# Performance work log

Measured on AMD Instinct MI355X. Metric: run time of the kernel, lower is better.

Reference implementation:

```python
import jax, jax.numpy as jnp
import numpy as np

B, T, E, H, D_PRICE = 16, 2048, 128, 4, 512


def setup_inputs() -> dict:
    key = jax.random.key(0)
    ks = jax.random.split(key, 22)
    f32 = jnp.float32

    def w(k, shape):
        fan_in = shape[0]
        return (jax.random.normal(k, shape, f32) / np.sqrt(fan_in)).astype(f32)

    def b(k, n):
        return (jax.random.normal(k, (n,), f32) * 0.01).astype(f32)

    inp = {
        # OHLC prices, positive, normalized scale
        "ohlc": jax.random.uniform(ks[0], (B, T, 4), f32, 0.5, 1.5),
        # ohlc_proj: Linear(4, 64)
        "Wp": w(ks[1], (4, 64)), "bp": b(ks[2], 64),
        # curvature_net: Linear(64,128) -> ReLU -> Linear(128,32)
        "Wc1": w(ks[3], (64, 128)), "bc1": b(ks[4], 128),
        "Wc2": w(ks[5], (128, 32)), "bc2": b(ks[6], 32),
        # volatility_net: Linear(64,64) -> ReLU -> Linear(64,16)
        "Wv1": w(ks[7], (64, 64)), "bv1": b(ks[8], 64),
        "Wv2": w(ks[9], (64, 16)), "bv2": b(ks[10], 16),
        # sr_field_net: Linear(64,64) -> ReLU -> Linear(64,16)
        "Ws1": w(ks[11], (64, 64)), "bs1": b(ks[12], 64),
        "Ws2": w(ks[13], (64, 16)), "bs2": b(ks[14], 16),
        # MultiheadAttention(embed_dim=128, num_heads=4): fused in-proj + out-proj
        "Wqkv": w(ks[15], (E, 3 * E)), "bqkv": b(ks[16], 3 * E),
        "Wo": w(ks[17], (E, E)), "bo": b(ks[18], E),
        # output_proj: Linear(128, d_price)
        "Wout": w(ks[19], (E, D_PRICE)), "bout": b(ks[20], D_PRICE),
    }
    return inp


def _mlp(x, W1, b1, W2, b2):
    return jax.nn.relu(x @ W1 + b1) @ W2 + b2


def reference(ohlc, Wp, bp, Wc1, bc1, Wc2, bc2, Wv1, bv1, Wv2, bv2,
              Ws1, bs1, Ws2, bs2, Wqkv, bqkv, Wo, bo, Wout, bout):
    # NB: compute_curvature / compute_volatility_surface / detect_sr_levels
    # in the original forward are dead code (results never used), so they are
    # omitted here; output math is identical.
    e = ohlc @ Wp + bp                                   # [B,T,64]
    feats = jnp.concatenate([
        e,
        _mlp(e, Wc1, bc1, Wc2, bc2),                     # [B,T,32]
        _mlp(e, Wv1, bv1, Wv2, bv2),                     # [B,T,16]
        _mlp(e, Ws1, bs1, Ws2, bs2),                     # [B,T,16]
    ], axis=-1)                                          # [B,T,128]

    Bn, Tn, En = feats.shape
    dh = En // H
    qkv = feats @ Wqkv + bqkv                            # [B,T,3E]
    q, k, v = jnp.split(qkv, 3, axis=-1)

    def heads(x):
        return x.reshape(Bn, Tn, H, dh).transpose(0, 2, 1, 3)  # [B,H,T,dh]

    q, k, v = heads(q), heads(k), heads(v)
    scores = jnp.einsum('bhqd,bhkd->bhqk', q, k) / np.sqrt(dh).astype(feats.dtype)
    a = jax.nn.softmax(scores, axis=-1)                  # [B,H,T,T]
    o = jnp.einsum('bhqk,bhkd->bhqd', a, v)
    o = o.transpose(0, 2, 1, 3).reshape(Bn, Tn, En)
    attended = o @ Wo + bo                               # [B,T,128]

    pooled = attended.mean(axis=1)                       # [B,128]
    return pooled @ Wout + bout                          # [B,512]
```

## Files before the change

kernel.cpp:

```cpp
#include <hip/hip_runtime.h>


typedef __attribute__((ext_vector_type(4)))  float f32x4;
typedef __attribute__((ext_vector_type(16))) float f32x16;
typedef __attribute__((ext_vector_type(4)))  short short4v;
typedef __attribute__((ext_vector_type(8)))  short short8v;

static __device__ __forceinline__ unsigned short f2b(float f) {
    unsigned int u = __builtin_bit_cast(unsigned int, f);
    u += 0x7fffu + ((u >> 16) & 1u);
    return (unsigned short)(u >> 16);
}

static __device__ __forceinline__ unsigned int cvtpk_bf16(float a, float b) {
    unsigned int r;
    asm volatile("v_cvt_pk_bf16_f32 %0, %1, %2" : "=v"(r) : "v"(a), "v"(b));
    return r;
}

__global__ __launch_bounds__(256) void prep_kernel(
    const float* Wqkv, const float* Wc1, const float* Wc2, const float* Wv1,
    const float* Wv2, const float* Ws1, const float* Ws2,
    unsigned short* wqkvt, unsigned short* wc1t, unsigned short* wc2t,
    unsigned short* wv1t, unsigned short* wv2t, unsigned short* ws1t,
    unsigned short* ws2t, float* pooled, float* qkmax)
{
    int tid = threadIdx.x;
    if (blockIdx.x < 48) {
        __shared__ float tile[32][33];
        int bidn = blockIdx.x % 12, bidk = blockIdx.x / 12;
        int n0 = bidn * 32, k0 = bidk * 32;
        {
            int r = tid >> 3, cq = tid & 7;
            float4 v = *(const float4*)(Wqkv + (size_t)(k0 + r) * 384 + n0 + cq * 4);
            tile[r][cq*4+0] = v.x; tile[r][cq*4+1] = v.y;
            tile[r][cq*4+2] = v.z; tile[r][cq*4+3] = v.w;
        }
        __syncthreads();
        {
            int nr = tid >> 3, kq = tid & 7;
            union { unsigned short us[4]; short4v v; } pk;
#pragma unroll
            for (int j = 0; j < 4; ++j) pk.us[j] = f2b(tile[kq*4+j][nr]);
            *(short4v*)(wqkvt + (size_t)(n0 + nr) * 128 + k0 + kq * 4) = pk.v;
        }
        return;
    }
    int idx = (blockIdx.x - 48) * 256 + tid;
    if (idx < 8192)  { int n = idx >> 6, kk = idx & 63;  wc1t[idx] = f2b(Wc1[kk*128 + n]); return; }
    idx -= 8192;
    if (idx < 4096)  { int n = idx >> 7, kk = idx & 127; wc2t[idx] = f2b(Wc2[kk*32  + n]); return; }
    idx -= 4096;
    if (idx < 4096)  { int n = idx >> 6, kk = idx & 63;  wv1t[idx] = f2b(Wv1[kk*64  + n]); return; }
    idx -= 4096;
    if (idx < 1024)  { int n = idx >> 6, kk = idx & 63;  wv2t[idx] = f2b(Wv2[kk*16  + n]); return; }
    idx -= 1024;
    if (idx < 4096)  { int n = idx >> 6, kk = idx & 63;  ws1t[idx] = f2b(Ws1[kk*64  + n]); return; }
    idx -= 4096;
    if (idx < 1024)  { int n = idx >> 6, kk = idx & 63;  ws2t[idx] = f2b(Ws2[kk*16  + n]); return; }
    idx -= 1024;
    if (idx < 2048)  { pooled[idx] = 0.f; return; }
    idx -= 2048;
    if (idx < 128)   qkmax[idx] = 0.f;
}

template<int N, int K, int A_ROWB, bool RELU, bool TO_LDS>
static __device__ __forceinline__ void tile_gemm(
    const char* As, const unsigned short* __restrict__ BT,
    const float* __restrict__ bias, char* Ht,
    unsigned short* __restrict__ gOut, int ocol,
    int m0, int w, int lane)
{
    constexpr int ASL = A_ROWB / 16, NT = N / 16, KS = K / 32;
    int l15 = lane & 15, hi4 = lane >> 4;
    f32x4 acc[NT];
#pragma unroll
    for (int nt = 0; nt < NT; ++nt)
#pragma unroll
        for (int r = 0; r < 4; ++r) acc[nt][r] = 0.f;

#pragma unroll
    for (int ks = 0; ks < KS; ++ks) {
        int slot = ks * 4 + hi4;
        int m = w * 16 + l15;
        short8v af = *(const short8v*)(As + m * A_ROWB + ((slot ^ (m & (ASL - 1))) << 4));
#pragma unroll
        for (int nt = 0; nt < NT; ++nt) {
            int n = nt * 16 + l15;
            short8v bf = *(const short8v*)(BT + (size_t)n * K + slot * 8);
            acc[nt] = __builtin_amdgcn_mfma_f32_16x16x32_bf16(af, bf, acc[nt], 0, 0, 0);
        }
    }
#pragma unroll
    for (int nt = 0; nt < NT; ++nt) {
        int n = nt * 16 + l15;
        float bv = bias[n];
#pragma unroll
        for (int r = 0; r < 4; ++r) {
            int m = w * 16 + hi4 * 4 + r;
            float v = acc[nt][r] + bv;
            if (RELU) v = fmaxf(v, 0.f);
            if (TO_LDS) {
                *(unsigned short*)(Ht + m * 256 + ((((n >> 3) ^ (m & 15))) << 4) + (n & 7) * 2) = f2b(v);
            } else {
                gOut[(size_t)(m0 + m) * 128 + ocol + n] = f2b(v);
            }
        }
    }
}

__global__ __launch_bounds__(256) void fused_mlp(
    const float* __restrict__ ohlc, const float* __restrict__ Wp, const float* __restrict__ bp,
    const unsigned short* __restrict__ wc1t, const float* __restrict__ bc1,
    const unsigned short* __restrict__ wc2t, const float* __restrict__ bc2,
    const unsigned short* __restrict__ wv1t, const float* __restrict__ bv1,
    const unsigned short* __restrict__ wv2t, const float* __restrict__ bv2,
    const unsigned short* __restrict__ ws1t, const float* __restrict__ bs1,
    const unsigned short* __restrict__ ws2t, const float* __restrict__ bs2,
    unsigned short* __restrict__ feats)
{
    __shared__ float wp[256];
    __shared__ float bpl[64];
    __shared__ char Et[64 * 128];
    __shared__ char Ht[64 * 256];

    int tid = threadIdx.x;
    int m0 = blockIdx.x * 64;
    wp[tid] = Wp[tid];
    if (tid < 64) bpl[tid] = bp[tid];
    __syncthreads();

    {
        int tok = tid >> 2, jq = tid & 3;
        float4 ov = ((const float4*)ohlc)[m0 + tok];
#pragma unroll
        for (int c = 0; c < 2; ++c) {
            int sl = jq * 2 + c;
            union { unsigned short us[8]; short8v v; } pk;
#pragma unroll
            for (int jj = 0; jj < 8; ++jj) {
                int j = sl * 8 + jj;
                float e = bpl[j] + ov.x * wp[j] + ov.y * wp[64 + j]
                                 + ov.z * wp[128 + j] + ov.w * wp[192 + j];
                pk.us[jj] = f2b(e);
            }
            *(short8v*)(Et + tok * 128 + ((sl ^ (tok & 7)) << 4)) = pk.v;
            *(short8v*)(feats + (size_t)(m0 + tok) * 128 + sl * 8) = pk.v;
        }
    }
    __syncthreads();

    int lane = tid & 63, w = tid >> 6;
    tile_gemm<128, 64, 128, true,  true >(Et, wc1t, bc1, Ht, feats, 0,   m0, w, lane);
    tile_gemm<32, 128, 256, false, false>(Ht, wc2t, bc2, Ht, feats, 64,  m0, w, lane);
    tile_gemm<64,  64, 128, true,  true >(Et, wv1t, bv1, Ht, feats, 0,   m0, w, lane);
    tile_gemm<16,  64, 256, false, false>(Ht, wv2t, bv2, Ht, feats, 96,  m0, w, lane);
    tile_gemm<64,  64, 128, true,  true >(Et, ws1t, bs1, Ht, feats, 0,   m0, w, lane);
    tile_gemm<16,  64, 256, false, false>(Ht, ws2t, bs2, Ht, feats, 112, m0, w, lane);
}

__global__ __launch_bounds__(256) void qkv_gemm(
    const unsigned short* __restrict__ feats,
    const unsigned short* __restrict__ wqkvt, const float* __restrict__ bqkv,
    unsigned short* __restrict__ qg, unsigned short* __restrict__ kg,
    unsigned short* __restrict__ vt2, float* __restrict__ qkmax)
{
    constexpr int ROWB = 256, CPR = 16;
    __shared__ short8v smemv[4096];
    char* As = (char*)smemv;
    char* Bs = (char*)smemv + 32768;

    int tid = threadIdx.x;
    int m0 = blockIdx.x * 128;
    int sel = blockIdx.y;
    const unsigned short* BT = wqkvt + (size_t)sel * 128 * 128;

    for (int c = tid; c < 128 * CPR; c += 256) {
        int m = c / CPR, s = c % CPR;
        short8v v = *(const short8v*)(feats + (size_t)(m0 + m) * 128 + s * 8);
        *(short8v*)(As + m * ROWB + ((s ^ (m & 15)) * 16)) = v;
    }
    for (int c = tid; c < 128 * CPR; c += 256) {
        int n = c / CPR, s = c % CPR;
        short8v v = *(const short8v*)(BT + (size_t)n * 128 + s * 8);
        *(short8v*)(Bs + n * ROWB + ((s ^ (n & 15)) * 16)) = v;
    }
    __syncthreads();

    int lane = tid & 63, w = tid >> 6;
    int l15 = lane & 15, hi4 = lane >> 4;

    f32x4 acc[2][8];
#pragma unroll
    for (int mt = 0; mt < 2; ++mt)
#pragma unroll
        for (int nt = 0; nt < 8; ++nt)
#pragma unroll
            for (int r = 0; r < 4; ++r) acc[mt][nt][r] = 0.f;

#pragma unroll
    for (int ks = 0; ks < 4; ++ks) {
        int slot = ks * 4 + hi4;
        short8v af[2];
#pragma unroll
        for (int mt = 0; mt < 2; ++mt) {
            int m = w * 32 + mt * 16 + l15;
            af[mt] = *(const short8v*)(As + m * ROWB + ((slot ^ (m & 15)) * 16));
        }
#pragma unroll
        for (int nt = 0; nt < 8; ++nt) {
            int n = nt * 16 + l15;
            short8v bf = *(const short8v*)(Bs + n * ROWB + ((slot ^ (n & 15)) * 16));
            acc[0][nt] = __builtin_amdgcn_mfma_f32_16x16x32_bf16(af[0], bf, acc[0][nt], 0, 0, 0);
            acc[1][nt] = __builtin_amdgcn_mfma_f32_16x16x32_bf16(af[1], bf, acc[1][nt], 0, 0, 0);
        }
    }

    const float QSCALE = 1.4426950408889634f * 0.17677669529663687f;
    int b = m0 >> 11, tp0 = m0 & 2047;

    if (sel == 2) {
#pragma unroll
        for (int mt = 0; mt < 2; ++mt)
#pragma unroll
            for (int nt = 0; nt < 8; ++nt) {
                int n = nt * 16 + l15;
                float bv = bqkv[256 + n];
                int h = n >> 5, dh = n & 31;
                uint2 pk;
                pk.x = cvtpk_bf16(acc[mt][nt][0] + bv, acc[mt][nt][1] + bv);
                pk.y = cvtpk_bf16(acc[mt][nt][2] + bv, acc[mt][nt][3] + bv);
                int g32 = (tp0 >> 5) + w;
                size_t o = (size_t)(b * 4 + h) * 65536 + (size_t)g32 * 1024
                         + dh * 32 + hi4 * 8 + mt * 4;
                *(uint2*)(vt2 + o) = pk;
            }
    } else {
        float amax[4] = {0.f, 0.f, 0.f, 0.f};
        float scale = (sel == 0) ? QSCALE : 1.0f;
#pragma unroll
        for (int mt = 0; mt < 2; ++mt)
#pragma unroll
            for (int nt = 0; nt < 8; ++nt) {
                int n = nt * 16 + l15;
                float bv = bqkv[sel * 128 + n];
#pragma unroll
                for (int r = 0; r < 4; ++r) {
                    float v = (acc[mt][nt][r] + bv) * scale;
                    amax[nt >> 1] = fmaxf(amax[nt >> 1], fabsf(v));
                    int m = w * 32 + mt * 16 + hi4 * 4 + r;
                    *(unsigned short*)(As + m * 256 + (((n >> 3) ^ (m & 7)) << 4) + (n & 7) * 2) = f2b(v);
                }
            }
#pragma unroll
        for (int g = 0; g < 4; ++g) {
            float mv = amax[g];
            mv = fmaxf(mv, __shfl_xor(mv, 1));  mv = fmaxf(mv, __shfl_xor(mv, 2));
            mv = fmaxf(mv, __shfl_xor(mv, 4));  mv = fmaxf(mv, __shfl_xor(mv, 8));
            mv = fmaxf(mv, __shfl_xor(mv, 16)); mv = fmaxf(mv, __shfl_xor(mv, 32));
            if (lane == 0)
                atomicMax((int*)(qkmax + sel * 64 + b * 4 + g), __float_as_int(mv));
        }
        __syncthreads();
        unsigned short* og = (sel == 0) ? qg : kg;
#pragma unroll
        for (int it = 0; it < 8; ++it) {
            int ch = it * 256 + tid;
            int m = ch >> 4, c = ch & 15;
            short8v vv = *(const short8v*)(As + m * 256 + ((c ^ (m & 7)) << 4));
            int h = c >> 2, dq = c & 3;
            *(short8v*)(og + ((size_t)(b * 4 + h) * 2048 + tp0 + m) * 32 + dq * 8) = vv;
        }
    }
}

__global__ __launch_bounds__(256, 2) void attn_kernel(
    const unsigned short* __restrict__ qg, const unsigned short* __restrict__ kg,
    const unsigned short* __restrict__ vt2, const float* __restrict__ qkmax,
    float* __restrict__ pooled)
{
    int tid = threadIdx.x, bid = blockIdx.x;
    int bh = bid & 63, qc = bid >> 6;
    int b = bh >> 2;
    int lane = tid & 63, w = tid >> 6;
    int l15 = lane & 15, h = (lane >> 4) & 3;
    int q0 = qc * 256 + w * 64;

    const char* qp = (const char*)qg + ((size_t)bh * 2048 + q0) * 64 + l15 * 64 + h * 16;
    short8v Qf[4];
#pragma unroll
    for (int j = 0; j < 4; ++j) Qf[j] = *(const short8v*)(qp + j * 1024);

    float negM0 = -(32.0f * qkmax[bh] * qkmax[64 + bh]);
    f32x4 NEGM4 = {negM0, negM0, negM0, negM0};

    f32x4 accO[4][2], lacc[4];
#pragma unroll
    for (int j = 0; j < 4; ++j) {
#pragma unroll
        for (int r = 0; r < 4; ++r) { accO[j][0][r] = 0.f; accO[j][1][r] = 0.f; lacc[j][r] = 0.f; }
    }

    short8v ONES;
    {
        union { unsigned short us[8]; short8v v; } u;
#pragma unroll
        for (int j = 0; j < 8; ++j) u.us[j] = 0x3F80;
        ONES = u.v;
    }

    const char* kc = (const char*)kg  + (size_t)bh * 131072 + l15 * 64 + h * 16;
    const char* vc = (const char*)vt2 + (size_t)bh * 131072 + l15 * 64 + h * 16;

    auto compute = [&](short8v Ka, short8v Kb, short8v Va, short8v Vb) {
        union { unsigned int u[4]; short8v v; } pk[4];
#pragma unroll
        for (int tau = 0; tau < 2; ++tau) {
            short8v Kf = tau ? Kb : Ka;
#pragma unroll
            for (int j = 0; j < 4; ++j) {
                f32x4 s = __builtin_amdgcn_mfma_f32_16x16x32_bf16(Kf, Qf[j], NEGM4, 0, 0, 0);
                float p0 = __builtin_amdgcn_exp2f(s[0]);
                float p1 = __builtin_amdgcn_exp2f(s[1]);
                float p2 = __builtin_amdgcn_exp2f(s[2]);
                float p3 = __builtin_amdgcn_exp2f(s[3]);
                pk[j].u[tau * 2 + 0] = cvtpk_bf16(p0, p1);
                pk[j].u[tau * 2 + 1] = cvtpk_bf16(p2, p3);
            }
        }
#pragma unroll
        for (int j = 0; j < 4; ++j) {
            lacc[j]    = __builtin_amdgcn_mfma_f32_16x16x32_bf16(ONES, pk[j].v, lacc[j], 0, 0, 0);
            accO[j][0] = __builtin_amdgcn_mfma_f32_16x16x32_bf16(Va,   pk[j].v, accO[j][0], 0, 0, 0);
            accO[j][1] = __builtin_amdgcn_mfma_f32_16x16x32_bf16(Vb,   pk[j].v, accO[j][1], 0, 0, 0);
        }
    };

    short8v KaE, KbE, VaE, VbE, KaO, KbO, VaO, VbO;
    KaE = *(const short8v*)(kc);
    KbE = *(const short8v*)(kc + 1024);
    VaE = *(const short8v*)(vc);
    VbE = *(const short8v*)(vc + 1024);

#pragma unroll 1
    for (int g = 0; g < 64; g += 2) {
        {
            const char* kn = kc + (size_t)(g + 1) * 2048;
            const char* vn = vc + (size_t)(g + 1) * 2048;
            KaO = *(const short8v*)(kn);
            KbO = *(const short8v*)(kn + 1024);
            VaO = *(const short8v*)(vn);
            VbO = *(const short8v*)(vn + 1024);
        }
        compute(KaE, KbE, VaE, VbE);
        if (g + 2 < 64) {
            const char* kn = kc + (size_t)(g + 2) * 2048;
            const char* vn = vc + (size_t)(g + 2) * 2048;
            KaE = *(const short8v*)(kn);
            KbE = *(const short8v*)(kn + 1024);
            VaE = *(const short8v*)(vn);
            VbE = *(const short8v*)(vn + 1024);
        }
        compute(KaO, KbO, VaO, VbO);
    }

    float o8[2][4];
#pragma unroll
    for (int d = 0; d < 2; ++d)
#pragma unroll
        for (int r = 0; r < 4; ++r) o8[d][r] = 0.f;
#pragma unroll
    for (int j = 0; j < 4; ++j) {
        float inv = 1.0f / (lacc[j][0] + 1e-30f);
#pragma unroll
        for (int d = 0; d < 2; ++d)
#pragma unroll
            for (int r = 0; r < 4; ++r) o8[d][r] += accO[j][d][r] * inv;
    }
#pragma unroll
    for (int d = 0; d < 2; ++d)
#pragma unroll
        for (int r = 0; r < 4; ++r) {
            float v = o8[d][r];
            v += __shfl_xor(v, 1); v += __shfl_xor(v, 2);
            v += __shfl_xor(v, 4); v += __shfl_xor(v, 8);
            if (l15 == 0) {
                int dh = d * 16 + h * 4 + r;
                atomicAdd(pooled + b * 128 + (bh & 3) * 32 + dh, v);
            }
        }
}

__global__ __launch_bounds__(256) void head_kernel(
    const float* __restrict__ pooled, const float* __restrict__ Wo,
    const float* __restrict__ bo, const float* __restrict__ Wout,
    const float* __restrict__ bout, float* __restrict__ out)
{
    int bq = blockIdx.x, tid = threadIdx.x;
    __shared__ float pl[128], mid[128];
    if (tid < 128) pl[tid] = pooled[bq * 128 + tid] * (1.f / 2048.f);
    __syncthreads();
    if (tid < 128) {
        float s = bo[tid];
#pragma unroll 4
        for (int c = 0; c < 128; ++c) s += pl[c] * Wo[c * 128 + tid];
        mid[tid] = s;
    }
    __syncthreads();
    for (int j = tid; j < 512; j += 256) {
        float s = bout[j];
#pragma unroll 4
        for (int i = 0; i < 128; ++i) s += mid[i] * Wout[i * 512 + j];
        out[bq * 512 + j] = s;
    }
}

extern "C" void kernel_launch(void* const* d_in, const int* in_sizes, int n_in,
                              void* d_out, int out_size, void* d_ws, size_t ws_size,
                              hipStream_t stream) {
    (void)in_sizes; (void)n_in; (void)out_size; (void)ws_size;
    const float* ohlc = (const float*)d_in[0];
    const float* Wp   = (const float*)d_in[1];  const float* bp   = (const float*)d_in[2];
    const float* Wc1  = (const float*)d_in[3];  const float* bc1  = (const float*)d_in[4];
    const float* Wc2  = (const float*)d_in[5];  const float* bc2  = (const float*)d_in[6];
    const float* Wv1  = (const float*)d_in[7];  const float* bv1  = (const float*)d_in[8];
    const float* Wv2  = (const float*)d_in[9];  const float* bv2  = (const float*)d_in[10];
    const float* Ws1  = (const float*)d_in[11]; const float* bs1  = (const float*)d_in[12];
    const float* Ws2  = (const float*)d_in[13]; const float* bs2  = (const float*)d_in[14];
    const float* Wqkv = (const float*)d_in[15]; const float* bqkv = (const float*)d_in[16];
    const float* Wo   = (const float*)d_in[17]; const float* bo   = (const float*)d_in[18];
    const float* Wout = (const float*)d_in[19]; const float* bout = (const float*)d_in[20];
    float* out = (float*)d_out;
    char* ws = (char*)d_ws;

    const size_t MB8 = 8388608;
    unsigned short* feats = (unsigned short*)(ws);
    unsigned short* qg    = (unsigned short*)(ws + 1 * MB8);
    unsigned short* kg    = (unsigned short*)(ws + 2 * MB8);
    unsigned short* vt2   = (unsigned short*)(ws + 3 * MB8);
    float*          pooled = (float*)(ws + 4 * MB8);
    float*          qkmax  = (float*)(ws + 4 * MB8 + 8192);
    unsigned short* wc1t  = (unsigned short*)(ws + 4 * MB8 + 8192 + 512);
    unsigned short* wc2t  = wc1t + 8192;
    unsigned short* wv1t  = wc2t + 4096;
    unsigned short* wv2t  = wv1t + 4096;
    unsigned short* ws1t  = wv2t + 1024;
    unsigned short* ws2t  = ws1t + 4096;
    unsigned short* wqkvt = ws2t + 1024;

    prep_kernel<<<145, 256, 0, stream>>>(Wqkv, Wc1, Wc2, Wv1, Wv2, Ws1, Ws2,
                                         wqkvt, wc1t, wc2t, wv1t, wv2t, ws1t, ws2t,
                                         pooled, qkmax);
    fused_mlp<<<512, 256, 0, stream>>>(ohlc, Wp, bp, wc1t, bc1, wc2t, bc2,
                                       wv1t, bv1, wv2t, bv2, ws1t, bs1, ws2t, bs2, feats);
    qkv_gemm<<<dim3(256, 3), 256, 0, stream>>>(feats, wqkvt, bqkv, qg, kg, vt2, qkmax);
    attn_kernel<<<512, 256, 0, stream>>>(qg, kg, vt2, qkmax, pooled);
    head_kernel<<<16, 256, 0, stream>>>(pooled, Wo, bo, Wout, bout, out);
}
```

Measured before the change: 130.0 us.

## Stage K/V tiles through shared LDS double buffer with 8 waves per attention block

The attention kernel now uses 512 threads per block, each wave handling 32 queries instead of 64. The block cooperatively loads each K/V chunk once into a double-buffered LDS tile, with register prefetch and a barrier per chunk, rather than every wave reading K/V from global memory on its own. This cuts redundant global/L2 traffic and per-wave register pressure, at the cost of two barriers per iteration. The MLP kernel also gets separate LDS hidden buffers for each branch, so the three first-layer GEMMs can run back to back before the second-layer GEMMs.

Result: no change. 131.4 us (+1.1%).

```diff
diff --git a/kernel.cpp b/kernel.cpp
--- a/kernel.cpp
+++ b/kernel.cpp
@@ -2,7 +2,6 @@
 
 
 typedef __attribute__((ext_vector_type(4)))  float f32x4;
-typedef __attribute__((ext_vector_type(16))) float f32x16;
 typedef __attribute__((ext_vector_type(4)))  short short4v;
 typedef __attribute__((ext_vector_type(8)))  short short8v;
 
@@ -64,14 +63,15 @@
     if (idx < 128)   qkmax[idx] = 0.f;
 }
 
-template<int N, int K, int A_ROWB, bool RELU, bool TO_LDS>
+template<int N, int K, int A_ROWB, int D_ROWB, bool RELU, bool TO_LDS>
 static __device__ __forceinline__ void tile_gemm(
     const char* As, const unsigned short* __restrict__ BT,
-    const float* __restrict__ bias, char* Ht,
+    const float* __restrict__ bias, char* dst,
     unsigned short* __restrict__ gOut, int ocol,
     int m0, int w, int lane)
 {
-    constexpr int ASL = A_ROWB / 16, NT = N / 16, KS = K / 32;
+    constexpr int ASL = A_ROWB / 16, DSL = D_ROWB / 16;
+    constexpr int NT = N / 16, KS = K / 32;
     int l15 = lane & 15, hi4 = lane >> 4;
     f32x4 acc[NT];
 #pragma unroll
@@ -101,7 +101,8 @@
             float v = acc[nt][r] + bv;
             if (RELU) v = fmaxf(v, 0.f);
             if (TO_LDS) {
-                *(unsigned short*)(Ht + m * 256 + ((((n >> 3) ^ (m & 15))) << 4) + (n & 7) * 2) = f2b(v);
+                int col = n;
+                *(unsigned short*)(dst + m * D_ROWB + (((col >> 3) ^ (m & (DSL - 1))) << 4) + (col & 7) * 2) = f2b(v);
             } else {
                 gOut[(size_t)(m0 + m) * 128 + ocol + n] = f2b(v);
             }
@@ -122,7 +123,9 @@
     __shared__ float wp[256];
     __shared__ float bpl[64];
     __shared__ char Et[64 * 128];
-    __shared__ char Ht[64 * 256];
+    __shared__ char Hc[64 * 256];
+    __shared__ char Hv[64 * 128];
+    __shared__ char Hs[64 * 128];
 
     int tid = threadIdx.x;
     int m0 = blockIdx.x * 64;
@@ -151,12 +154,12 @@
     __syncthreads();
 
     int lane = tid & 63, w = tid >> 6;
-    tile_gemm<128, 64, 128, true,  true >(Et, wc1t, bc1, Ht, feats, 0,   m0, w, lane);
-    tile_gemm<32, 128, 256, false, false>(Ht, wc2t, bc2, Ht, feats, 64,  m0, w, lane);
-    tile_gemm<64,  64, 128, true,  true >(Et, wv1t, bv1, Ht, feats, 0,   m0, w, lane);
-    tile_gemm<16,  64, 256, false, false>(Ht, wv2t, bv2, Ht, feats, 96,  m0, w, lane);
-    tile_gemm<64,  64, 128, true,  true >(Et, ws1t, bs1, Ht, feats, 0,   m0, w, lane);
-    tile_gemm<16,  64, 256, false, false>(Ht, ws2t, bs2, Ht, feats, 112, m0, w, lane);
+    tile_gemm<128, 64, 128, 256, true, true >(Et, wc1t, bc1, Hc, feats, 0, m0, w, lane);
+    tile_gemm< 64, 64, 128, 128, true, true >(Et, wv1t, bv1, Hv, feats, 0, m0, w, lane);
+    tile_gemm< 64, 64, 128, 128, true, true >(Et, ws1t, bs1, Hs, feats, 0, m0, w, lane);
+    tile_gemm< 32, 128, 256, 256, false, false>(Hc, wc2t, bc2, Hc, feats, 64,  m0, w, lane);
+    tile_gemm< 16,  64, 128, 128, false, false>(Hv, wv2t, bv2, Hv, feats, 96,  m0, w, lane);
+    tile_gemm< 16,  64, 128, 128, false, false>(Hs, ws2t, bs2, Hs, feats, 112, m0, w, lane);
 }
 
 __global__ __launch_bounds__(256) void qkv_gemm(
@@ -274,32 +277,33 @@
     }
 }
 
-__global__ __launch_bounds__(256, 2) void attn_kernel(
+__global__ __launch_bounds__(512) void attn_kernel(
     const unsigned short* __restrict__ qg, const unsigned short* __restrict__ kg,
     const unsigned short* __restrict__ vt2, const float* __restrict__ qkmax,
     float* __restrict__ pooled)
 {
+    __shared__ char Kv[2][4096];
+
     int tid = threadIdx.x, bid = blockIdx.x;
     int bh = bid & 63, qc = bid >> 6;
     int b = bh >> 2;
     int lane = tid & 63, w = tid >> 6;
     int l15 = lane & 15, h = (lane >> 4) & 3;
-    int q0 = qc * 256 + w * 64;
+    int q0 = qc * 256 + w * 32;
 
     const char* qp = (const char*)qg + ((size_t)bh * 2048 + q0) * 64 + l15 * 64 + h * 16;
-    short8v Qf[4];
-#pragma unroll
-    for (int j = 0; j < 4; ++j) Qf[j] = *(const short8v*)(qp + j * 1024);
+    short8v Qf[2];
+    Qf[0] = *(const short8v*)(qp);
+    Qf[1] = *(const short8v*)(qp + 1024);
 
     float negM0 = -(32.0f * qkmax[bh] * qkmax[64 + bh]);
     f32x4 NEGM4 = {negM0, negM0, negM0, negM0};
 
-    f32x4 accO[4][2], lacc[4];
-#pragma unroll
-    for (int j = 0; j < 4; ++j) {
+    f32x4 accO[2][2], lacc[2];
+#pragma unroll
+    for (int j = 0; j < 2; ++j)
 #pragma unroll
         for (int r = 0; r < 4; ++r) { accO[j][0][r] = 0.f; accO[j][1][r] = 0.f; lacc[j][r] = 0.f; }
-    }
 
     short8v ONES;
     {
@@ -309,16 +313,23 @@
         ONES = u.v;
     }
 
-    const char* kc = (const char*)kg  + (size_t)bh * 131072 + l15 * 64 + h * 16;
-    const char* vc = (const char*)vt2 + (size_t)bh * 131072 + l15 * 64 + h * 16;
-
-    auto compute = [&](short8v Ka, short8v Kb, short8v Va, short8v Vb) {
-        union { unsigned int u[4]; short8v v; } pk[4];
+    const char* gk = (const char*)kg  + (size_t)bh * 131072;
+    const char* gv = (const char*)vt2 + (size_t)bh * 131072;
+    const char* gsrc = (tid < 256) ? (gk + (tid & 255) * 8) : (gv + (tid & 255) * 8);
+    int ldst = (tid < 256) ? (tid * 8) : (2048 + (tid - 256) * 8);
+    int foff = l15 * 64 + h * 16;
+
+    auto compute = [&](const char* bufp) {
+        short8v Ka = *(const short8v*)(bufp + foff);
+        short8v Kb = *(const short8v*)(bufp + 1024 + foff);
+        short8v Va = *(const short8v*)(bufp + 2048 + foff);
+        short8v Vb = *(const short8v*)(bufp + 3072 + foff);
+        union { unsigned int u[4]; short8v v; } pk[2];
 #pragma unroll
         for (int tau = 0; tau < 2; ++tau) {
             short8v Kf = tau ? Kb : Ka;
 #pragma unroll
-            for (int j = 0; j < 4; ++j) {
+            for (int j = 0; j < 2; ++j) {
                 f32x4 s = __builtin_amdgcn_mfma_f32_16x16x32_bf16(Kf, Qf[j], NEGM4, 0, 0, 0);
                 float p0 = __builtin_amdgcn_exp2f(s[0]);
                 float p1 = __builtin_amdgcn_exp2f(s[1]);
@@ -329,39 +340,29 @@
             }
         }
 #pragma unroll
-        for (int j = 0; j < 4; ++j) {
+        for (int j = 0; j < 2; ++j) {
             lacc[j]    = __builtin_amdgcn_mfma_f32_16x16x32_bf16(ONES, pk[j].v, lacc[j], 0, 0, 0);
             accO[j][0] = __builtin_amdgcn_mfma_f32_16x16x32_bf16(Va,   pk[j].v, accO[j][0], 0, 0, 0);
             accO[j][1] = __builtin_amdgcn_mfma_f32_16x16x32_bf16(Vb,   pk[j].v, accO[j][1], 0, 0, 0);
         }
     };
 
-    short8v KaE, KbE, VaE, VbE, KaO, KbO, VaO, VbO;
-    KaE = *(const short8v*)(kc);
-    KbE = *(const short8v*)(kc + 1024);
-    VaE = *(const short8v*)(vc);
-    VbE = *(const short8v*)(vc + 1024);
+    uint2 R;
+    R = *(const uint2*)(gsrc);
+    *(uint2*)(Kv[0] + ldst) = R;
+    R = *(const uint2*)(gsrc + 2048);
+    __syncthreads();
 
 #pragma unroll 1
     for (int g = 0; g < 64; g += 2) {
-        {
-            const char* kn = kc + (size_t)(g + 1) * 2048;
-            const char* vn = vc + (size_t)(g + 1) * 2048;
-            KaO = *(const short8v*)(kn);
-            KbO = *(const short8v*)(kn + 1024);
-            VaO = *(const short8v*)(vn);
-            VbO = *(const short8v*)(vn + 1024);
-        }
-        compute(KaE, KbE, VaE, VbE);
-        if (g + 2 < 64) {
-            const char* kn = kc + (size_t)(g + 2) * 2048;
-            const char* vn = vc + (size_t)(g + 2) * 2048;
-            KaE = *(const short8v*)(kn);
-            KbE = *(const short8v*)(kn + 1024);
-            VaE = *(const short8v*)(vn);
-            VbE = *(const short8v*)(vn + 1024);
-        }
-        compute(KaO, KbO, VaO, VbO);
+        *(uint2*)(Kv[1] + ldst) = R;
+        if (g + 2 < 64) R = *(const uint2*)(gsrc + (size_t)(g + 2) * 2048);
+        compute(Kv[0]);
+        __syncthreads();
+        if (g + 2 < 64) *(uint2*)(Kv[0] + ldst) = R;
+        if (g + 3 < 64) R = *(const uint2*)(gsrc + (size_t)(g + 3) * 2048);
+        compute(Kv[1]);
+        __syncthreads();
     }
 
     float o8[2][4];
@@ -370,7 +371,7 @@
 #pragma unroll
         for (int r = 0; r < 4; ++r) o8[d][r] = 0.f;
 #pragma unroll
-    for (int j = 0; j < 4; ++j) {
+    for (int j = 0; j < 2; ++j) {
         float inv = 1.0f / (lacc[j][0] + 1e-30f);
 #pragma unroll
         for (int d = 0; d < 2; ++d)
@@ -454,6 +455,6 @@
     fused_mlp<<<512, 256, 0, stream>>>(ohlc, Wp, bp, wc1t, bc1, wc2t, bc2,
                                        wv1t, bv1, wv2t, bv2, ws1t, bs1, ws2t, bs2, feats);
     qkv_gemm<<<dim3(256, 3), 256, 0, stream>>>(feats, wqkvt, bqkv, qg, kg, vt2, qkmax);
-    attn_kernel<<<512, 256, 0, stream>>>(qg, kg, vt2, qkmax, pooled);
+    attn_kernel<<<512, 512, 0, stream>>>(qg, kg, vt2, qkmax, pooled);
     head_kernel<<<16, 256, 0, stream>>>(pooled, Wo, bo, Wout, bout, out);
 }
```
